# Kernel optimization log

Measured on AMD Instinct MI355X. Metric: run time of the kernel, lower is better.

The kernel has to match this reference:

```python
import jax, jax.numpy as jnp
import numpy as np

EPS = 1e-5

def _bn2d(z, gamma, beta):
    # training-mode BatchNorm2d: stats over (B,H,W), biased variance
    mean = jnp.mean(z, axis=(0, 2, 3), keepdims=True)
    var = jnp.var(z, axis=(0, 2, 3), keepdims=True)
    return (z - mean) / jnp.sqrt(var + EPS) * gamma[None, :, None, None] + beta[None, :, None, None]

def _conv1x1(z, w):
    # 1x1 conv, no bias: w is [out_c, in_c]
    return jnp.einsum('bchw,oc->bohw', z, w)

def setup_inputs() -> dict:
    key = jax.random.key(0)
    ks = jax.random.split(key, 16)
    B, C, H, W, NC = 8, 64, 64, 64, 100
    inter = C // 2
    inp = {
        'x': jax.random.normal(ks[0], (B, C, H, W), jnp.float32),
        'y': jax.random.normal(ks[1], (B, C, H, W), jnp.float32),
        'logitx': jax.random.normal(ks[2], (B, NC), jnp.float32),
        'logity': jax.random.normal(ks[3], (B, NC), jnp.float32),
        'conv1_w': jax.random.normal(ks[4], (C, 2 * C), jnp.float32) * 0.05,
        'conv1_b': jnp.zeros((C,), jnp.float32),
        'bn1_g': jnp.ones((C,), jnp.float32),
        'bn1_b': jnp.zeros((C,), jnp.float32),
        'phi_w': jax.random.normal(ks[5], (inter, C), jnp.float32) * 0.05,
        'theta_w': jax.random.normal(ks[6], (inter, C), jnp.float32) * 0.05,
        'g_w': jax.random.normal(ks[7], (inter, C), jnp.float32) * 0.05,
        'mask_w': jax.random.normal(ks[8], (C, inter), jnp.float32) * 0.05,
        'fc_w': jax.random.normal(ks[9], (2, C), jnp.float32) * 0.05,
        'fc_b': jnp.zeros((2,), jnp.float32),
        'bnv_g': jnp.ones((2,), jnp.float32),
        'bnv_b': jnp.zeros((2,), jnp.float32),
    }
    return inp

def reference(x, y, logitx, logity, conv1_w, conv1_b, bn1_g, bn1_b,
              phi_w, theta_w, g_w, mask_w, fc_w, fc_b, bnv_g, bnv_b):
    b, c, h, w = x.shape  # c == 64
    inter = c // 2
    # conv1 + bn1
    feasc = jnp.concatenate([x, y], axis=1)
    feasc = jnp.einsum('bchw,oc->bohw', feasc, conv1_w) + conv1_b[None, :, None, None]
    feasc = _bn2d(feasc, bn1_g, bn1_b)
    # NonLocalBlockND(64): note the faithful view quirk —
    # conv outputs inter=32 channels but is reshaped as (b, c=64, h*w//2)
    N = h * w // 2
    x_phi = _conv1x1(feasc, phi_w).reshape(b, c, N)            # (b, 64, N)
    x_theta = _conv1x1(feasc, theta_w).reshape(b, c, N)        # (b, 64, N)
    x_theta = jnp.swapaxes(x_theta, 1, 2)                      # (b, N, 64)
    x_g = jnp.swapaxes(_conv1x1(feasc, g_w).reshape(b, c, N), 1, 2)  # (b, N, 64)
    attn = jnp.einsum('bnc,bcm->bnm', x_theta, x_phi)          # (b, N, N)
    attn = jax.nn.softmax(attn, axis=1)                        # non-standard softmax axis (dim=1)
    o = jnp.einsum('bnm,bmc->bnc', attn, x_g)                  # (b, N, 64)
    o = jnp.swapaxes(o, 1, 2).reshape(b, inter, h, w)          # (b, 32, h, w)
    mask = _conv1x1(o, mask_w)                                 # (b, 64, h, w)
    feasc = mask + feasc
    # gating head
    feas = jnp.mean(feasc, axis=(2, 3))                        # (b, 64) adaptive avg pool
    feas = feas @ fc_w.T + fc_b                                # (b, 2)
    # training-mode BatchNorm1d over batch dim
    mean = jnp.mean(feas, axis=0, keepdims=True)
    var = jnp.var(feas, axis=0, keepdims=True)
    feas = (feas - mean) / jnp.sqrt(var + EPS) * bnv_g[None, :] + bnv_b[None, :]
    feas = jax.nn.softmax(jax.nn.relu(feas), axis=1)
    logit = feas[:, 0:1] * logitx + feas[:, 1:2] * logity
    return feasc, logit
```

## Files before the change

### kernel.cpp

```cpp
#include <hip/hip_runtime.h>

#define CH 64
#define HW 4096
#define NN 2048

typedef __attribute__((ext_vector_type(8))) short bf8_t;
typedef __attribute__((ext_vector_type(4))) float f4_t;
#define MFMA16 __builtin_amdgcn_mfma_f32_16x16x32_bf16
#define LOG2E 1.4426950408889634f

static __device__ inline unsigned short f2bf(float f) {
  union { float f; unsigned u; } v; v.f = f;
  unsigned r = v.u + 0x7fff + ((v.u >> 16) & 1);
  return (unsigned short)(r >> 16);
}
static __device__ inline float bf2f(unsigned short u) {
  union { unsigned u; float f; } v; v.u = ((unsigned)u) << 16;
  return v.f;
}

__global__ __launch_bounds__(256) void k_conv1(const float* __restrict__ x,
    const float* __restrict__ y, const float* __restrict__ w,
    const float* __restrict__ bias, float* __restrict__ z,
    float2* __restrict__ partials) {
  __shared__ float wl[128][32];
  __shared__ float redS[4][32], redQ[4][32];
  int t = threadIdx.x;
  int yh = blockIdx.y;
  int bx = blockIdx.x;
  for (int i = t; i < 4096; i += 256) {
    int o = i & 31, c = i >> 5;
    wl[c][o] = w[(yh * 32 + o) * 128 + c];
  }
  __syncthreads();
  int b = bx >> 4;
  int s = ((bx & 15) << 8) + t;
  const float* xb = x + b * (CH * HW) + s;
  const float* yb = y + b * (CH * HW) + s;
  float acc[32];
#pragma unroll
  for (int o = 0; o < 32; ++o) acc[o] = 0.f;
  for (int c0 = 0; c0 < 64; c0 += 16) {
    float xr[16], yr[16];
#pragma unroll
    for (int j = 0; j < 16; ++j) {
      xr[j] = xb[(c0 + j) * HW];
      yr[j] = yb[(c0 + j) * HW];
    }
#pragma unroll
    for (int j = 0; j < 16; ++j) {
      int c = c0 + j;
      const float4* wx = reinterpret_cast<const float4*>(&wl[c][0]);
      const float4* wy = reinterpret_cast<const float4*>(&wl[c + 64][0]);
#pragma unroll
      for (int o4 = 0; o4 < 8; ++o4) {
        float4 a = wx[o4], bb = wy[o4];
        acc[4 * o4 + 0] += xr[j] * a.x + yr[j] * bb.x;
        acc[4 * o4 + 1] += xr[j] * a.y + yr[j] * bb.y;
        acc[4 * o4 + 2] += xr[j] * a.z + yr[j] * bb.z;
        acc[4 * o4 + 3] += xr[j] * a.w + yr[j] * bb.w;
      }
    }
  }
  float* zb = z + b * (CH * HW) + s;
  int lane = t & 63, wv = t >> 6;
#pragma unroll
  for (int o = 0; o < 32; ++o) {
    float v = acc[o] + bias[yh * 32 + o];
    zb[(yh * 32 + o) * HW] = v;
    float a1 = v, a2 = v * v;
    for (int off = 32; off; off >>= 1) {
      a1 += __shfl_xor(a1, off);
      a2 += __shfl_xor(a2, off);
    }
    if (lane == 0) { redS[wv][o] = a1; redQ[wv][o] = a2; }
  }
  __syncthreads();
  if (t < 32) {
    float2 pp;
    pp.x = redS[0][t] + redS[1][t] + redS[2][t] + redS[3][t];
    pp.y = redQ[0][t] + redQ[1][t] + redQ[2][t] + redQ[3][t];
    partials[((bx << 1) + yh) * 32 + t] = pp;
  }
}

__global__ __launch_bounds__(256) void k_prep1(const float2* __restrict__ partials,
    const float* __restrict__ phw, const float* __restrict__ thw,
    const float* __restrict__ gw, const float* __restrict__ mask_w,
    const float* __restrict__ g1, const float* __restrict__ b1,
    float* __restrict__ effw, float* __restrict__ effb,
    unsigned short* __restrict__ wMbf, float* __restrict__ scA,
    float* __restrict__ shA) {
  __shared__ float scS[64], shS[64];
  int t = threadIdx.x;
  if (t < 64) {
    int yh = t >> 5, o = t & 31;
    float S = 0.f, S2 = 0.f;
    for (int cb = 0; cb < 128; ++cb) {
      float2 p = partials[((cb << 1) + yh) * 32 + o];
      S += p.x; S2 += p.y;
    }
    float mean = S * (1.f / 32768.f);
    float var = S2 * (1.f / 32768.f) - mean * mean;
    float is = rsqrtf(var + 1e-5f);
    float sc = g1[t] * is;
    float sh = b1[t] - mean * sc;
    scS[t] = sc; shS[t] = sh;
    scA[t] = sc; shA[t] = sh;
  }
  __syncthreads();
  for (int i = t; i < 6144; i += 256) {
    int p = i >> 11, c = (i >> 5) & 63, ic = i & 31;
    const float* wp = (p == 0) ? phw : (p == 1) ? thw : gw;
    float scale = (p == 1) ? LOG2E : 1.0f;
    effw[i] = wp[ic * 64 + c] * scS[c] * scale;
  }
  for (int i = t; i < 2048; i += 256)
    wMbf[i] = f2bf(mask_w[i]);
  if (t < 96) {
    int p = t >> 5, ic = t & 31;
    const float* wp = (p == 0) ? phw : (p == 1) ? thw : gw;
    float scale = (p == 1) ? LOG2E : 1.0f;
    float s_ = 0.f;
    for (int c = 0; c < 64; ++c) s_ += wp[ic * 64 + c] * shS[c];
    effb[t] = s_ * scale;
  }
}

__global__ __launch_bounds__(256) void k_proj(const float* __restrict__ z,
    const float* __restrict__ effw, const float* __restrict__ effb,
    unsigned short* __restrict__ phiT, unsigned short* __restrict__ thetaT,
    unsigned short* __restrict__ gB) {
  int t = threadIdx.x;
  int p = blockIdx.y >> 1;
  int ih = blockIdx.y & 1;
  int bx = blockIdx.x;
  int b = bx >> 4;
  int s = ((bx & 15) << 8) + t;
  int n = s & 2047, hi = s >> 11;
  const float* zb = z + b * (CH * HW) + s;
  const float* wp = effw + p * 2048 + ih * 16;
  float acc[16];
#pragma unroll
  for (int j = 0; j < 16; ++j) acc[j] = effb[p * 32 + ih * 16 + j];
  for (int c0 = 0; c0 < 64; c0 += 16) {
    float zr[16];
#pragma unroll
    for (int j = 0; j < 16; ++j) zr[j] = zb[(c0 + j) * HW];
#pragma unroll
    for (int j = 0; j < 16; ++j) {
      const float4* w4 = reinterpret_cast<const float4*>(wp + (c0 + j) * 32);
#pragma unroll
      for (int q = 0; q < 4; ++q) {
        float4 wv = w4[q];
        acc[4 * q + 0] += zr[j] * wv.x;
        acc[4 * q + 1] += zr[j] * wv.y;
        acc[4 * q + 2] += zr[j] * wv.z;
        acc[4 * q + 3] += zr[j] * wv.w;
      }
    }
  }
  if (p < 2) {
    unsigned short* ob = (p == 0 ? phiT : thetaT) + b * (NN * 64) + n * 64 + hi * 32 + ih * 16;
    unsigned int pk[8];
#pragma unroll
    for (int q = 0; q < 8; ++q)
      pk[q] = (unsigned int)f2bf(acc[2 * q]) | ((unsigned int)f2bf(acc[2 * q + 1]) << 16);
    uint4* o4 = reinterpret_cast<uint4*>(ob);
    o4[0] = make_uint4(pk[0], pk[1], pk[2], pk[3]);
    o4[1] = make_uint4(pk[4], pk[5], pk[6], pk[7]);
  } else {
    unsigned short* ob = gB + b * (64 * NN) + n;
#pragma unroll
    for (int j = 0; j < 16; ++j) ob[(2 * (ih * 16 + j) + hi) * NN] = f2bf(acc[j]);
  }
}

__global__ __launch_bounds__(256) void k_colsum(const unsigned short* __restrict__ thetaT,
    const unsigned short* __restrict__ phiT, float* __restrict__ csum) {
  int bx = blockIdx.x;
  int b = blockIdx.y;
  int mtile = bx >> 2, nq = bx & 3;
  int m0 = mtile << 6;
  int t = threadIdx.x; int lane = t & 63; int w = t >> 6;
  const unsigned short* pT = phiT + b * (NN * 64);
  const unsigned short* tT = thetaT + b * (NN * 64);
  int l15 = lane & 15, lg = lane >> 4;
  __shared__ unsigned short thS[64][72];
  __shared__ float red[4][4][16];
  int srow = t >> 2, spart = t & 3;
  bf8_t bf[4][2];
#pragma unroll
  for (int mt = 0; mt < 4; ++mt)
#pragma unroll
    for (int kh = 0; kh < 2; ++kh)
      bf[mt][kh] = *(const bf8_t*)(pT + (m0 + 16 * mt + l15) * 64 + kh * 32 + lg * 8);
  float cs[4] = {0.f, 0.f, 0.f, 0.f};
  for (int nt = nq * 8; nt < nq * 8 + 8; ++nt) {
    __syncthreads();
    {
      const uint4* gt = reinterpret_cast<const uint4*>(tT + (nt * 64 + srow) * 64 + spart * 16);
      uint4* lt = reinterpret_cast<uint4*>(&thS[srow][spart * 16]);
      lt[0] = gt[0];
      lt[1] = gt[1];
    }
    __syncthreads();
    bf8_t a0 = *(const bf8_t*)&thS[w * 16 + l15][lg * 8];
    bf8_t a1 = *(const bf8_t*)&thS[w * 16 + l15][32 + lg * 8];
#pragma unroll
    for (int mt = 0; mt < 4; ++mt) {
      f4_t d = {0.f, 0.f, 0.f, 0.f};
      d = MFMA16(a0, bf[mt][0], d, 0, 0, 0);
      d = MFMA16(a1, bf[mt][1], d, 0, 0, 0);
      cs[mt] += __builtin_amdgcn_exp2f(d[0]) + __builtin_amdgcn_exp2f(d[1]) +
                __builtin_amdgcn_exp2f(d[2]) + __builtin_amdgcn_exp2f(d[3]);
    }
  }
#pragma unroll
  for (int mt = 0; mt < 4; ++mt) {
    float v = cs[mt];
    v += __shfl_xor(v, 16);
    v += __shfl_xor(v, 32);
    if (lane < 16) red[w][mt][lane] = v;
  }
  __syncthreads();
  if (t < 64) {
    int mt = t >> 4, col = t & 15;
    float s = red[0][mt][col] + red[1][mt][col] + red[2][mt][col] + red[3][mt][col];
    csum[b * 8192 + nq * 2048 + m0 + mt * 16 + col] = s;
  }
}

__global__ __launch_bounds__(256) void k_gscale(const float* __restrict__ csum,
    unsigned short* __restrict__ gB) {
  int bx = blockIdx.x;
  int b = bx >> 6, c = bx & 63;
  int t = threadIdx.x;
  int m = t * 8;
  const float* cs = csum + b * 8192;
  unsigned short* g = gB + b * (64 * NN) + c * NN + m;
  float r[8];
#pragma unroll
  for (int j = 0; j < 8; ++j) {
    float s = cs[m + j] + cs[2048 + m + j] + cs[4096 + m + j] + cs[6144 + m + j];
    r[j] = 1.f / s;
  }
  uint4 gv = *(const uint4*)g;
  unsigned int* gd = (unsigned int*)&gv;
  uint4 out;
  unsigned int* od = (unsigned int*)&out;
#pragma unroll
  for (int q = 0; q < 4; ++q) {
    float lo = bf2f((unsigned short)(gd[q] & 0xffff)) * r[2 * q];
    float hi = bf2f((unsigned short)(gd[q] >> 16)) * r[2 * q + 1];
    od[q] = (unsigned int)f2bf(lo) | ((unsigned int)f2bf(hi) << 16);
  }
  *(uint4*)g = out;
}

__global__ __launch_bounds__(256) void k_pv(const unsigned short* __restrict__ thetaT,
    const unsigned short* __restrict__ phiT, const unsigned short* __restrict__ gB,
    unsigned short* __restrict__ obufP) {
  int bx = blockIdx.x;
  int b = blockIdx.y;
  int ntile = bx >> 2, mq = bx & 3;
  int n0 = ntile << 6;
  int t = threadIdx.x; int lane = t & 63; int w = t >> 6;
  int l15 = lane & 15, lg = lane >> 4;
  const unsigned short* tT = thetaT + b * (NN * 64);
  const unsigned short* pT = phiT + b * (NN * 64);
  const unsigned short* gb = gB + b * (64 * NN);
  __shared__ unsigned short phiS[64][72];
  __shared__ unsigned short gS[64][72];
  __shared__ unsigned int P_u[4][16][33];
  int nrow = n0 + 16 * w + l15;
  bf8_t at0 = *(const bf8_t*)(tT + nrow * 64 + lg * 8);
  bf8_t at1 = *(const bf8_t*)(tT + nrow * 64 + 32 + lg * 8);
  int srow = t >> 2, spart = t & 3;
  f4_t oacc[4];
#pragma unroll
  for (int ct = 0; ct < 4; ++ct) oacc[ct] = (f4_t){0.f, 0.f, 0.f, 0.f};
  for (int mi = 0; mi < 8; ++mi) {
    int m0 = (mq * 8 + mi) << 6;
    __syncthreads();
    {
      const uint4* gp = reinterpret_cast<const uint4*>(pT + (m0 + srow) * 64 + spart * 16);
      uint4* lp = reinterpret_cast<uint4*>(&phiS[srow][spart * 16]);
      lp[0] = gp[0];
      lp[1] = gp[1];
      const uint4* gg = reinterpret_cast<const uint4*>(gb + srow * NN + m0 + spart * 16);
      uint4* lg_ = reinterpret_cast<uint4*>(&gS[srow][spart * 16]);
      lg_[0] = gg[0];
      lg_[1] = gg[1];
    }
    __syncthreads();
#pragma unroll
    for (int mt = 0; mt < 4; ++mt) {
      bf8_t b0 = *(const bf8_t*)&phiS[16 * mt + l15][lg * 8];
      bf8_t b1 = *(const bf8_t*)&phiS[16 * mt + l15][32 + lg * 8];
      f4_t d = {0.f, 0.f, 0.f, 0.f};
      d = MFMA16(b0, at0, d, 0, 0, 0);
      d = MFMA16(b1, at1, d, 0, 0, 0);
      float e0 = __builtin_amdgcn_exp2f(d[0]);
      float e1 = __builtin_amdgcn_exp2f(d[1]);
      float e2 = __builtin_amdgcn_exp2f(d[2]);
      float e3 = __builtin_amdgcn_exp2f(d[3]);
      unsigned int p01, p23;
      asm("v_cvt_pk_bf16_f32 %0, %1, %2" : "=v"(p01) : "v"(e0), "v"(e1));
      asm("v_cvt_pk_bf16_f32 %0, %1, %2" : "=v"(p23) : "v"(e2), "v"(e3));
      P_u[w][l15][8 * mt + 2 * lg] = p01;
      P_u[w][l15][8 * mt + 2 * lg + 1] = p23;
    }
    bf8_t ap0 = *(const bf8_t*)&P_u[w][l15][4 * lg];
    bf8_t ap1 = *(const bf8_t*)&P_u[w][l15][16 + 4 * lg];
#pragma unroll
    for (int ct = 0; ct < 4; ++ct) {
      bf8_t g0 = *(const bf8_t*)&gS[16 * ct + l15][lg * 8];
      bf8_t g1 = *(const bf8_t*)&gS[16 * ct + l15][32 + lg * 8];
      oacc[ct] = MFMA16(ap0, g0, oacc[ct], 0, 0, 0);
      oacc[ct] = MFMA16(ap1, g1, oacc[ct], 0, 0, 0);
    }
  }
  unsigned short* ob = obufP + (mq * 8 + b) * 131072;
#pragma unroll
  for (int ct = 0; ct < 4; ++ct) {
    int c = 16 * ct + l15;
    int nb = n0 + 16 * w + lg * 4;
    int ic = c >> 1;
    int posb = (c & 1) * 2048 + nb;
#pragma unroll
    for (int q = 0; q < 4; ++q)
      ob[(posb + q) * 32 + ic] = f2bf(oacc[ct][q]);
  }
}

__global__ __launch_bounds__(256) void k_mask(const unsigned short* __restrict__ obufP,
    const unsigned short* __restrict__ wMbf, const float* __restrict__ scA,
    const float* __restrict__ shA, float* __restrict__ zio,
    float* __restrict__ poolpart) {
  __shared__ unsigned short wMl[64][40];
  __shared__ float red[4][4][16];
  int t = threadIdx.x, lane = t & 63, w = t >> 6;
  int l15 = lane & 15, lg = lane >> 4;
  int bx = blockIdx.x;
  int b = bx >> 6;
  int p0 = (bx & 63) * 64 + w * 16;
  {
    int row = t >> 2, part = t & 3;
    *(uint4*)&wMl[row][part * 8] = *(const uint4*)(wMbf + row * 32 + part * 8);
  }
  __syncthreads();
  bf8_t bw[4];
#pragma unroll
  for (int ct = 0; ct < 4; ++ct)
    bw[ct] = *(const bf8_t*)&wMl[16 * ct + l15][lg * 8];
  f4_t acc[4];
#pragma unroll
  for (int ct = 0; ct < 4; ++ct) acc[ct] = (f4_t){0.f, 0.f, 0.f, 0.f};
#pragma unroll
  for (int mq = 0; mq < 4; ++mq) {
    bf8_t a = *(const bf8_t*)(obufP + ((mq * 8 + b) << 17) + (p0 + l15) * 32 + lg * 8);
#pragma unroll
    for (int ct = 0; ct < 4; ++ct)
      acc[ct] = MFMA16(a, bw[ct], acc[ct], 0, 0, 0);
  }
  float* zb = zio + b * (CH * HW);
#pragma unroll
  for (int ct = 0; ct < 4; ++ct) {
    int oc = 16 * ct + l15;
    int pg = p0 + 4 * lg;
    float4 zv = *(const float4*)(zb + oc * HW + pg);
    float sc = scA[oc], sh = shA[oc];
    float4 r;
    r.x = acc[ct][0] + sc * zv.x + sh;
    r.y = acc[ct][1] + sc * zv.y + sh;
    r.z = acc[ct][2] + sc * zv.z + sh;
    r.w = acc[ct][3] + sc * zv.w + sh;
    *(float4*)(zb + oc * HW + pg) = r;
    float s = r.x + r.y + r.z + r.w;
    s += __shfl_xor(s, 16);
    s += __shfl_xor(s, 32);
    if (lg == 0) red[w][ct][l15] = s;
  }
  __syncthreads();
  if (t < 64) {
    int ct = t >> 4, cl = t & 15;
    poolpart[bx * 64 + ct * 16 + cl] =
        red[0][ct][cl] + red[1][ct][cl] + red[2][ct][cl] + red[3][ct][cl];
  }
}

__global__ __launch_bounds__(256) void k_head(const float* __restrict__ poolpart,
    const float* __restrict__ fcw, const float* __restrict__ fcb,
    const float* __restrict__ bg, const float* __restrict__ bb,
    const float* __restrict__ lx, const float* __restrict__ ly,
    float* __restrict__ outLogit) {
  __shared__ float poolS[8][64];
  __shared__ float fv[8][2];
  __shared__ float gate[8][2];
  int t = threadIdx.x;
  for (int idx = t; idx < 512; idx += 256) {
    int b = idx >> 6, oc = idx & 63;
    float s = 0.f;
    for (int ch = 0; ch < 64; ++ch)
      s += poolpart[((b << 6) + ch) * 64 + oc];
    poolS[b][oc] = s * (1.f / 4096.f);
  }
  __syncthreads();
  if (t < 16) {
    int b = t >> 1, k = t & 1;
    float s = fcb[k];
    for (int c = 0; c < 64; ++c) s += poolS[b][c] * fcw[k * 64 + c];
    fv[b][k] = s;
  }
  __syncthreads();
  if (t < 2) {
    float m = 0.f;
    for (int b = 0; b < 8; ++b) m += fv[b][t];
    m *= 0.125f;
    float v = 0.f;
    for (int b = 0; b < 8; ++b) { float d = fv[b][t] - m; v += d * d; }
    v *= 0.125f;
    float is = rsqrtf(v + 1e-5f);
    for (int b = 0; b < 8; ++b) gate[b][t] = bg[t] * (fv[b][t] - m) * is + bb[t];
  }
  __syncthreads();
  if (t < 8) {
    float a = fmaxf(gate[t][0], 0.f), b2 = fmaxf(gate[t][1], 0.f);
    float mx = fmaxf(a, b2);
    float e0 = __expf(a - mx), e1 = __expf(b2 - mx);
    float inv = 1.f / (e0 + e1);
    gate[t][0] = e0 * inv;
    gate[t][1] = e1 * inv;
  }
  __syncthreads();
  for (int i = t; i < 800; i += 256) {
    int b = i / 100;
    outLogit[i] = gate[b][0] * lx[i] + gate[b][1] * ly[i];
  }
}

extern "C" void kernel_launch(void* const* d_in, const int* in_sizes, int n_in,
                              void* d_out, int out_size, void* d_ws, size_t ws_size,
                              hipStream_t stream) {
  (void)in_sizes; (void)n_in; (void)out_size; (void)ws_size;
  const float* x = (const float*)d_in[0];
  const float* y = (const float*)d_in[1];
  const float* logitx = (const float*)d_in[2];
  const float* logity = (const float*)d_in[3];
  const float* conv1_w = (const float*)d_in[4];
  const float* conv1_b = (const float*)d_in[5];
  const float* bn1_g = (const float*)d_in[6];
  const float* bn1_b = (const float*)d_in[7];
  const float* phi_w = (const float*)d_in[8];
  const float* theta_w = (const float*)d_in[9];
  const float* g_w = (const float*)d_in[10];
  const float* mask_w = (const float*)d_in[11];
  const float* fc_w = (const float*)d_in[12];
  const float* fc_b = (const float*)d_in[13];
  const float* bnv_g = (const float*)d_in[14];
  const float* bnv_b = (const float*)d_in[15];

  unsigned short* U = (unsigned short*)d_ws;
  float* F = (float*)d_ws;
  unsigned short* thetaT = U;
  unsigned short* phiT   = U + 1048576;
  unsigned short* gB     = U + 2097152;
  unsigned short* obufP  = U + 3145728;
  float* csum      = F + 3670016;
  float* poolpart  = F + 3670016;
  float2* partials = (float2*)(F + 3735552);
  float* effw      = F + 3751936;
  float* effb      = F + 3758080;
  unsigned short* wMbf = (unsigned short*)(F + 3758208);
  float* scA       = F + 3759232;
  float* shA       = F + 3759296;

  float* zout = (float*)d_out;
  float* lout = zout + 2097152;

  k_conv1<<<dim3(128, 2), 256, 0, stream>>>(x, y, conv1_w, conv1_b, zout, partials);
  k_prep1<<<1, 256, 0, stream>>>(partials, phi_w, theta_w, g_w, mask_w,
                                 bn1_g, bn1_b, effw, effb, wMbf, scA, shA);
  k_proj<<<dim3(128, 6), 256, 0, stream>>>(zout, effw, effb, phiT, thetaT, gB);
  k_colsum<<<dim3(128, 8), 256, 0, stream>>>(thetaT, phiT, csum);
  k_gscale<<<512, 256, 0, stream>>>(csum, gB);
  k_pv<<<dim3(128, 8), 256, 0, stream>>>(thetaT, phiT, gB, obufP);
  k_mask<<<512, 256, 0, stream>>>(obufP, wMbf, scA, shA, zout, poolpart);
  k_head<<<1, 256, 0, stream>>>(poolpart, fc_w, fc_b, bnv_g, bnv_b, logitx, logity, lout);
}
```

Measured before the change: 142.6 us.

## Register-prefetch next phi/g tile and stage attention output through LDS

```diff
diff --git a/kernel.cpp b/kernel.cpp
--- a/kernel.cpp
+++ b/kernel.cpp
@@ -280,18 +280,24 @@
   f4_t oacc[4];
 #pragma unroll
   for (int ct = 0; ct < 4; ++ct) oacc[ct] = (f4_t){0.f, 0.f, 0.f, 0.f};
+  int m0p = (mq * 8) << 6;
+  uint4 rp0 = *(const uint4*)(pT + (m0p + srow) * 64 + spart * 16);
+  uint4 rp1 = *(const uint4*)(pT + (m0p + srow) * 64 + spart * 16 + 8);
+  uint4 rg0 = *(const uint4*)(gb + srow * NN + m0p + spart * 16);
+  uint4 rg1 = *(const uint4*)(gb + srow * NN + m0p + spart * 16 + 8);
   for (int mi = 0; mi < 8; ++mi) {
     int m0 = (mq * 8 + mi) << 6;
     __syncthreads();
-    {
-      const uint4* gp = reinterpret_cast<const uint4*>(pT + (m0 + srow) * 64 + spart * 16);
-      uint4* lp = reinterpret_cast<uint4*>(&phiS[srow][spart * 16]);
-      lp[0] = gp[0];
-      lp[1] = gp[1];
-      const uint4* gg = reinterpret_cast<const uint4*>(gb + srow * NN + m0 + spart * 16);
-      uint4* lg_ = reinterpret_cast<uint4*>(&gS[srow][spart * 16]);
-      lg_[0] = gg[0];
-      lg_[1] = gg[1];
+    *(uint4*)&phiS[srow][spart * 16] = rp0;
+    *(uint4*)&phiS[srow][spart * 16 + 8] = rp1;
+    *(uint4*)&gS[srow][spart * 16] = rg0;
+    *(uint4*)&gS[srow][spart * 16 + 8] = rg1;
+    if (mi < 7) {
+      int m1 = (mq * 8 + mi + 1) << 6;
+      rp0 = *(const uint4*)(pT + (m1 + srow) * 64 + spart * 16);
+      rp1 = *(const uint4*)(pT + (m1 + srow) * 64 + spart * 16 + 8);
+      rg0 = *(const uint4*)(gb + srow * NN + m1 + spart * 16);
+      rg1 = *(const uint4*)(gb + srow * NN + m1 + spart * 16 + 8);
     }
     __syncthreads();
 #pragma unroll
@@ -321,17 +327,25 @@
       oacc[ct] = MFMA16(ap1, g1, oacc[ct], 0, 0, 0);
     }
   }
-  unsigned short* ob = obufP + (mq * 8 + b) * 131072;
+  __syncthreads();
+  unsigned short* OT = (unsigned short*)&gS[0][0];
 #pragma unroll
   for (int ct = 0; ct < 4; ++ct) {
     int c = 16 * ct + l15;
-    int nb = n0 + 16 * w + lg * 4;
-    int ic = c >> 1;
-    int posb = (c & 1) * 2048 + nb;
+    int ph = c & 1, ic = c >> 1;
+    int rbase = ph * 64 + 16 * w + 4 * lg;
 #pragma unroll
     for (int q = 0; q < 4; ++q)
-      ob[(posb + q) * 32 + ic] = f2bf(oacc[ct][q]);
-  }
+      OT[(rbase + q) * 32 + ic] = f2bf(oacc[ct][q]);
+  }
+  __syncthreads();
+  unsigned short* ob = obufP + (mq * 8 + b) * 131072;
+  int r = t >> 1, hf = t & 1;
+  const uint4* src = (const uint4*)(OT + r * 32 + hf * 16);
+  int gpos = (r >> 6) * 2048 + n0 + (r & 63);
+  uint4* dst = (uint4*)(ob + gpos * 32 + hf * 16);
+  dst[0] = src[0];
+  dst[1] = src[1];
 }
 
 __global__ __launch_bounds__(256) void k_mask(const unsigned short* __restrict__ obufP,
```

New measurement: 142.7 us. No clear change (+0.0%).
